# Performance work log

Hardware: AMD Instinct MI355X
Metric: run time of the kernel (lower is better)

Reference implementation:

```python
import jax, jax.numpy as jnp
import numpy as np

N = 50000
E = 800000
IN_DIM = 256
HID = 128
OUT = 64


def setup_inputs() -> dict:
    key = jax.random.key(0)
    ks = jax.random.split(key, 12)
    inp = {}
    inp["x"] = jax.random.normal(ks[0], (N, IN_DIM), dtype=jnp.float32)
    inp["edge_index"] = jax.random.randint(ks[1], (2, E), 0, N, dtype=jnp.int64)
    s0 = 1.0 / np.sqrt(IN_DIM)
    inp["W0"] = jax.random.uniform(ks[2], (IN_DIM, HID), jnp.float32, -s0, s0)
    inp["b0"] = jax.random.uniform(ks[3], (HID,), jnp.float32, -s0, s0)
    sa = 1.0 / np.sqrt(2 * HID)
    inp["att_w1"] = jax.random.uniform(ks[4], (2 * HID, 1), jnp.float32, -sa, sa)
    inp["att_b1"] = jax.random.uniform(ks[5], (1,), jnp.float32, -sa, sa)
    inp["eps1"] = jnp.float32(0.1)
    inp["att_w2"] = jax.random.uniform(ks[6], (2 * HID, 1), jnp.float32, -sa, sa)
    inp["att_b2"] = jax.random.uniform(ks[7], (1,), jnp.float32, -sa, sa)
    inp["eps2"] = jnp.float32(0.1)
    sc = 1.0 / np.sqrt(HID)
    inp["Wc"] = jax.random.uniform(ks[8], (HID, OUT), jnp.float32, -sc, sc)
    inp["bc"] = jax.random.uniform(ks[9], (OUT,), jnp.float32, -sc, sc)
    return inp


def _fagcn_layer(x, row, col, att_w, att_b, eps):
    # x: [N, H]; row/col: [E]
    x_i = x[row]                       # [E, H] source (gathered)
    x_j = x[col]                       # [E, H] destination
    # cat([x_i, x_j]) @ att_w == x_i @ att_w[:H] + x_j @ att_w[H:]
    H = x.shape[1]
    score = x_i @ att_w[:H] + x_j @ att_w[H:] + att_b  # [E, 1]
    alpha = jnp.tanh(score)            # [E, 1]
    messages = alpha * x_i             # [E, H]
    agg = jax.ops.segment_sum(messages, col, num_segments=x.shape[0])  # [N, H]
    return eps * x + (1.0 - eps) * agg


def reference(x, edge_index, W0, b0, att_w1, att_b1, eps1, att_w2, att_b2, eps2, Wc, bc):
    row, col = edge_index[0], edge_index[1]
    h = jax.nn.relu(x @ W0 + b0)       # initial linear + relu (dropout=eval identity)
    h = jax.nn.relu(_fagcn_layer(h, row, col, att_w1, att_b1, eps1))
    h = jax.nn.relu(_fagcn_layer(h, row, col, att_w2, att_b2, eps2))
    return h @ Wc + bc                 # [N, OUT]
```

## Files before the change

### kernel.cpp

```cpp
#include <hip/hip_runtime.h>

#define N_NODES 50000
#define E_EDGES 800000
#define IN_DIM 256
#define HID 128
#define OUT_DIM 64

typedef unsigned short u16;
typedef __attribute__((ext_vector_type(8))) short short8;
typedef __attribute__((ext_vector_type(4))) float floatx4;

__device__ __forceinline__ u16 f2bf(float f) {
    unsigned u = __float_as_uint(f);
    unsigned r = (u + 0x7FFFu + ((u >> 16) & 1u)) >> 16;
    return (u16)r;
}
__device__ __forceinline__ void bf8_unpack(uint4 v, float* f) {
    f[0] = __uint_as_float(v.x << 16); f[1] = __uint_as_float(v.x & 0xffff0000u);
    f[2] = __uint_as_float(v.y << 16); f[3] = __uint_as_float(v.y & 0xffff0000u);
    f[4] = __uint_as_float(v.z << 16); f[5] = __uint_as_float(v.z & 0xffff0000u);
    f[6] = __uint_as_float(v.w << 16); f[7] = __uint_as_float(v.w & 0xffff0000u);
}
__device__ __forceinline__ uint4 bf8_pack(const float* f) {
    uint4 o;
    o.x = f2bf(f[0]) | ((unsigned)f2bf(f[1]) << 16);
    o.y = f2bf(f[2]) | ((unsigned)f2bf(f[3]) << 16);
    o.z = f2bf(f[4]) | ((unsigned)f2bf(f[5]) << 16);
    o.w = f2bf(f[6]) | ((unsigned)f2bf(f[7]) << 16);
    return o;
}

__global__ __launch_bounds__(256) void k_prep(const int* __restrict__ ei,
                                              int* __restrict__ cnt,
                                              int* __restrict__ rank,
                                              const float* __restrict__ W0,
                                              u16* __restrict__ Wt,
                                              const float* __restrict__ Wc,
                                              u16* __restrict__ Wct) {
    const int gid = blockIdx.x * 256 + threadIdx.x;
    if (gid < E_EDGES / 8) {
        const int4 c0 = ((const int4*)(ei + E_EDGES))[2 * gid];
        const int4 c1 = ((const int4*)(ei + E_EDGES))[2 * gid + 1];
        int4 r0, r1;
        r0.x = atomicAdd(&cnt[c0.x], 1);
        r0.y = atomicAdd(&cnt[c0.y], 1);
        r0.z = atomicAdd(&cnt[c0.z], 1);
        r0.w = atomicAdd(&cnt[c0.w], 1);
        r1.x = atomicAdd(&cnt[c1.x], 1);
        r1.y = atomicAdd(&cnt[c1.y], 1);
        r1.z = atomicAdd(&cnt[c1.z], 1);
        r1.w = atomicAdd(&cnt[c1.w], 1);
        ((int4*)rank)[2 * gid] = r0;
        ((int4*)rank)[2 * gid + 1] = r1;
    }
    if (gid < IN_DIM * HID) {
        Wt[gid] = f2bf(W0[(gid & 255) * HID + (gid >> 8)]);
    }
    if (gid < HID * OUT_DIM) {
        Wct[gid] = f2bf(Wc[(gid & 127) * OUT_DIM + (gid >> 7)]);
    }
}

__global__ __launch_bounds__(1024) void k_scanA(const int* __restrict__ cnt,
                                                int* __restrict__ ptr,
                                                int* __restrict__ btot) {
    __shared__ int wtot[16];
    __shared__ int wexc[16];
    const int t = threadIdx.x;
    const int lane = t & 63;
    const int wd = t >> 6;
    const int i = blockIdx.x * 1024 + t;
    int v = (i < N_NODES) ? cnt[i] : 0;
    const int orig = v;
    #pragma unroll
    for (int off = 1; off < 64; off <<= 1) {
        int y = __shfl_up(v, off);
        if (lane >= off) v += y;
    }
    if (lane == 63) wtot[wd] = v;
    __syncthreads();
    if (t < 16) {
        int w = wtot[t];
        #pragma unroll
        for (int off = 1; off < 16; off <<= 1) {
            int y = __shfl_up(w, off);
            if (t >= off) w += y;
        }
        wexc[t] = w - wtot[t];
    }
    __syncthreads();
    if (i < N_NODES) ptr[i] = wexc[wd] + (v - orig);
    if (t == 0) btot[blockIdx.x] = wexc[15] + wtot[15];
}

__global__ __launch_bounds__(64) void k_scanB(int* __restrict__ btot,
                                              int* __restrict__ ptr) {
    const int t = threadIdx.x;
    int v = (t < 49) ? btot[t] : 0;
    const int orig = v;
    #pragma unroll
    for (int off = 1; off < 64; off <<= 1) {
        int y = __shfl_up(v, off);
        if (t >= off) v += y;
    }
    if (t < 49) btot[t] = v - orig;
    if (t == 0) ptr[N_NODES] = E_EDGES;
}

__global__ __launch_bounds__(1024) void k_scanC(int* __restrict__ ptr,
                                                const int* __restrict__ btot) {
    const int i = blockIdx.x * 1024 + threadIdx.x;
    if (i < N_NODES) ptr[i] += btot[blockIdx.x];
}

__global__ __launch_bounds__(256) void k_scatter(const int* __restrict__ ei,
                                                 const int* __restrict__ rank,
                                                 const int* __restrict__ ptr,
                                                 int* __restrict__ srcidx) {
    const int gid = blockIdx.x * 256 + threadIdx.x;
    if (gid >= E_EDGES / 8) return;
    const int4 w0 = ((const int4*)ei)[2 * gid];
    const int4 w1 = ((const int4*)ei)[2 * gid + 1];
    const int4 c0 = ((const int4*)(ei + E_EDGES))[2 * gid];
    const int4 c1 = ((const int4*)(ei + E_EDGES))[2 * gid + 1];
    const int4 r0 = ((const int4*)rank)[2 * gid];
    const int4 r1 = ((const int4*)rank)[2 * gid + 1];
    const int p0 = ptr[c0.x] + r0.x;
    const int p1 = ptr[c0.y] + r0.y;
    const int p2 = ptr[c0.z] + r0.z;
    const int p3 = ptr[c0.w] + r0.w;
    const int p4 = ptr[c1.x] + r1.x;
    const int p5 = ptr[c1.y] + r1.y;
    const int p6 = ptr[c1.z] + r1.z;
    const int p7 = ptr[c1.w] + r1.w;
    srcidx[p0] = w0.x;
    srcidx[p1] = w0.y;
    srcidx[p2] = w0.z;
    srcidx[p3] = w0.w;
    srcidx[p4] = w1.x;
    srcidx[p5] = w1.y;
    srcidx[p6] = w1.z;
    srcidx[p7] = w1.w;
}

#define LROWS 128
#define KS 64
#define KP 72

__global__ __launch_bounds__(256) void k_lin_mfma(
    const float* __restrict__ x, const u16* __restrict__ Wt,
    const float* __restrict__ b0, const float* __restrict__ aw1,
    u16* __restrict__ h, float* __restrict__ sa, float* __restrict__ sb) {
    __shared__ u16 As[LROWS][KP];
    __shared__ u16 Bs[HID][KP];
    const int t = threadIdx.x;
    const int lane = t & 63;
    const int w = t >> 6;
    const int sub = lane & 15;
    const int quad = lane >> 4;
    const int row0 = blockIdx.x * LROWS;

    floatx4 acc0[8], acc1[8];
    #pragma unroll
    for (int i = 0; i < 8; ++i) {
        acc0[i] = (floatx4){0.f, 0.f, 0.f, 0.f};
        acc1[i] = (floatx4){0.f, 0.f, 0.f, 0.f};
    }

    const int sr = t >> 1;
    const int sk = (t & 1) * 32;

    for (int k0 = 0; k0 < IN_DIM; k0 += KS) {
        {
            int gr = row0 + sr;
            if (gr > N_NODES - 1) gr = N_NODES - 1;
            const float* src = x + (size_t)gr * IN_DIM + k0 + sk;
            #pragma unroll
            for (int i = 0; i < 4; ++i) {
                float4 f0 = ((const float4*)src)[2 * i];
                float4 f1 = ((const float4*)src)[2 * i + 1];
                uint4 p;
                p.x = f2bf(f0.x) | ((unsigned)f2bf(f0.y) << 16);
                p.y = f2bf(f0.z) | ((unsigned)f2bf(f0.w) << 16);
                p.z = f2bf(f1.x) | ((unsigned)f2bf(f1.y) << 16);
                p.w = f2bf(f1.z) | ((unsigned)f2bf(f1.w) << 16);
                *(uint4*)&As[sr][sk + 8 * i] = p;
            }
            const u16* wsrc = Wt + sr * IN_DIM + k0 + sk;
            #pragma unroll
            for (int i = 0; i < 4; ++i)
                *(uint4*)&Bs[sr][sk + 8 * i] = ((const uint4*)wsrc)[i];
        }
        __syncthreads();
        #pragma unroll
        for (int kk = 0; kk < KS; kk += 32) {
            short8 a0 = *(const short8*)&As[w * 32 + sub][kk + quad * 8];
            short8 a1 = *(const short8*)&As[w * 32 + 16 + sub][kk + quad * 8];
            #pragma unroll
            for (int ct = 0; ct < 8; ++ct) {
                short8 bb = *(const short8*)&Bs[ct * 16 + sub][kk + quad * 8];
                acc0[ct] = __builtin_amdgcn_mfma_f32_16x16x32_bf16(a0, bb, acc0[ct], 0, 0, 0);
                acc1[ct] = __builtin_amdgcn_mfma_f32_16x16x32_bf16(a1, bb, acc1[ct], 0, 0, 0);
            }
        }
        __syncthreads();
    }

    float bias[8], w1c[8], w2c[8];
    #pragma unroll
    for (int ct = 0; ct < 8; ++ct) {
        const int col = ct * 16 + sub;
        bias[ct] = b0[col];
        w1c[ct] = aw1[col];
        w2c[ct] = aw1[HID + col];
    }
    float ps[2][4], pd[2][4];
    #pragma unroll
    for (int i = 0; i < 2; ++i)
        #pragma unroll
        for (int j = 0; j < 4; ++j) { ps[i][j] = 0.f; pd[i][j] = 0.f; }

    #pragma unroll
    for (int tile = 0; tile < 2; ++tile) {
        #pragma unroll
        for (int reg = 0; reg < 4; ++reg) {
            const int gr = row0 + w * 32 + tile * 16 + quad * 4 + reg;
            const bool ok = gr < N_NODES;
            #pragma unroll
            for (int ct = 0; ct < 8; ++ct) {
                floatx4 v = tile ? acc1[ct] : acc0[ct];
                const float val = fmaxf(v[reg] + bias[ct], 0.f);
                if (ok) h[(size_t)gr * HID + ct * 16 + sub] = f2bf(val);
                ps[tile][reg] += val * w1c[ct];
                pd[tile][reg] += val * w2c[ct];
            }
        }
    }
    #pragma unroll
    for (int tile = 0; tile < 2; ++tile) {
        #pragma unroll
        for (int reg = 0; reg < 4; ++reg) {
            float a = ps[tile][reg], d = pd[tile][reg];
            #pragma unroll
            for (int off = 1; off < 16; off <<= 1) {
                a += __shfl_xor(a, off);
                d += __shfl_xor(d, off);
            }
            if (sub == 0) {
                const int gr = row0 + w * 32 + tile * 16 + quad * 4 + reg;
                if (gr < N_NODES) { sa[gr] = a; sb[gr] = d; }
            }
        }
    }
}

__global__ __launch_bounds__(256) void k_agg(const u16* __restrict__ hin,
                                             const float* __restrict__ sa,
                                             const float* __restrict__ sb,
                                             const float* __restrict__ attb,
                                             const float* __restrict__ epsp,
                                             const int* __restrict__ ptr,
                                             const int* __restrict__ srcidx,
                                             u16* __restrict__ hout,
                                             const float* __restrict__ attw_next,
                                             float* __restrict__ sa_next,
                                             float* __restrict__ sb_next) {
    const int qid = threadIdx.x >> 4;
    const int sub = threadIdx.x & 15;
    const int n = blockIdx.x * 16 + qid;
    if (n >= N_NODES) return;
    const float b = attb[0];
    const float sbn = sb[n];
    const int beg = ptr[n];
    const int end = ptr[n + 1];
    float acc[8];
    #pragma unroll
    for (int j = 0; j < 8; ++j) acc[j] = 0.f;

    int e = beg;
    for (; e + 8 <= end; e += 8) {
        int s[8];
        #pragma unroll
        for (int i = 0; i < 8; ++i) s[i] = srcidx[e + i];
        uint4 v[8];
        #pragma unroll
        for (int i = 0; i < 8; ++i)
            v[i] = *(const uint4*)(hin + (size_t)s[i] * HID + sub * 8);
        float al[8];
        #pragma unroll
        for (int i = 0; i < 8; ++i) al[i] = tanhf(sa[s[i]] + sbn + b);
        #pragma unroll
        for (int i = 0; i < 8; ++i) {
            float f[8];
            bf8_unpack(v[i], f);
            #pragma unroll
            for (int j = 0; j < 8; ++j) acc[j] += al[i] * f[j];
        }
    }
    for (; e < end; ++e) {
        const int s = srcidx[e];
        const float a = tanhf(sa[s] + sbn + b);
        const uint4 v = *(const uint4*)(hin + (size_t)s * HID + sub * 8);
        float f[8];
        bf8_unpack(v, f);
        #pragma unroll
        for (int j = 0; j < 8; ++j) acc[j] += a * f[j];
    }

    const float eps = epsp[0];
    const float om = 1.f - eps;
    const uint4 sv = *(const uint4*)(hin + (size_t)n * HID + sub * 8);
    float self[8], hv[8];
    bf8_unpack(sv, self);
    #pragma unroll
    for (int j = 0; j < 8; ++j)
        hv[j] = fmaxf(eps * self[j] + om * acc[j], 0.f);
    *(uint4*)(hout + (size_t)n * HID + sub * 8) = bf8_pack(hv);

    if (attw_next != nullptr) {
        float psum = 0.f, dsum = 0.f;
        #pragma unroll
        for (int j = 0; j < 8; ++j) {
            psum += hv[j] * attw_next[sub * 8 + j];
            dsum += hv[j] * attw_next[HID + sub * 8 + j];
        }
        #pragma unroll
        for (int off = 1; off < 16; off <<= 1) {
            psum += __shfl_xor(psum, off);
            dsum += __shfl_xor(dsum, off);
        }
        if (sub == 0) { sa_next[n] = psum; sb_next[n] = dsum; }
    }
}

__global__ __launch_bounds__(256) void k_out_mfma(const u16* __restrict__ h,
                                                  const u16* __restrict__ Wct,
                                                  const float* __restrict__ bc,
                                                  float* __restrict__ out) {
    const int t = threadIdx.x;
    const int lane = t & 63;
    const int w = t >> 6;
    const int sub = lane & 15;
    const int quad = lane >> 4;
    const int row0 = blockIdx.x * 128 + w * 32;

    floatx4 acc[2][4];
    #pragma unroll
    for (int i = 0; i < 2; ++i)
        #pragma unroll
        for (int j = 0; j < 4; ++j) acc[i][j] = (floatx4){0.f, 0.f, 0.f, 0.f};

    int r0 = row0 + sub;      if (r0 > N_NODES - 1) r0 = N_NODES - 1;
    int r1 = row0 + 16 + sub; if (r1 > N_NODES - 1) r1 = N_NODES - 1;

    #pragma unroll
    for (int ks = 0; ks < 4; ++ks) {
        const int ko = ks * 32 + quad * 8;
        short8 a0 = *(const short8*)(h + (size_t)r0 * HID + ko);
        short8 a1 = *(const short8*)(h + (size_t)r1 * HID + ko);
        #pragma unroll
        for (int ct = 0; ct < 4; ++ct) {
            short8 bb = *(const short8*)(Wct + (ct * 16 + sub) * HID + ko);
            acc[0][ct] = __builtin_amdgcn_mfma_f32_16x16x32_bf16(a0, bb, acc[0][ct], 0, 0, 0);
            acc[1][ct] = __builtin_amdgcn_mfma_f32_16x16x32_bf16(a1, bb, acc[1][ct], 0, 0, 0);
        }
    }

    #pragma unroll
    for (int ct = 0; ct < 4; ++ct) {
        const float bias = bc[ct * 16 + sub];
        #pragma unroll
        for (int tile = 0; tile < 2; ++tile) {
            #pragma unroll
            for (int reg = 0; reg < 4; ++reg) {
                const int gr = row0 + tile * 16 + quad * 4 + reg;
                if (gr < N_NODES)
                    out[(size_t)gr * OUT_DIM + ct * 16 + sub] = acc[tile][ct][reg] + bias;
            }
        }
    }
}

extern "C" void kernel_launch(void* const* d_in, const int* in_sizes, int n_in,
                              void* d_out, int out_size, void* d_ws, size_t ws_size,
                              hipStream_t stream) {
    const float* x   = (const float*)d_in[0];
    const int*   ei  = (const int*)d_in[1];
    const float* W0  = (const float*)d_in[2];
    const float* b0  = (const float*)d_in[3];
    const float* aw1 = (const float*)d_in[4];
    const float* ab1 = (const float*)d_in[5];
    const float* e1  = (const float*)d_in[6];
    const float* aw2 = (const float*)d_in[7];
    const float* ab2 = (const float*)d_in[8];
    const float* e2  = (const float*)d_in[9];
    const float* Wc  = (const float*)d_in[10];
    const float* bc  = (const float*)d_in[11];
    float* out = (float*)d_out;

    u16* hA  = (u16*)d_ws;
    u16* hB  = hA + (size_t)N_NODES * HID;
    u16* Wt  = hB + (size_t)N_NODES * HID;
    u16* Wct = Wt + IN_DIM * HID;
    float* sa1 = (float*)(Wct + HID * OUT_DIM);
    float* sb1 = sa1 + N_NODES;
    float* sa2 = sb1 + N_NODES;
    float* sb2 = sa2 + N_NODES;
    int* cnt    = (int*)(sb2 + N_NODES);
    int* ptr    = cnt + N_NODES;
    int* srcidx = ptr + N_NODES + 1;
    int* rank   = srcidx + E_EDGES;
    int* btot   = rank + E_EDGES;

    hipMemsetAsync(cnt, 0, N_NODES * sizeof(int), stream);
    k_prep<<<(E_EDGES / 8 + 255) / 256, 256, 0, stream>>>(ei, cnt, rank, W0, Wt, Wc, Wct);
    k_scanA<<<(N_NODES + 1023) / 1024, 1024, 0, stream>>>(cnt, ptr, btot);
    k_scanB<<<1, 64, 0, stream>>>(btot, ptr);
    k_scanC<<<(N_NODES + 1023) / 1024, 1024, 0, stream>>>(ptr, btot);
    k_scatter<<<(E_EDGES / 8 + 255) / 256, 256, 0, stream>>>(ei, rank, ptr, srcidx);

    k_lin_mfma<<<(N_NODES + LROWS - 1) / LROWS, 256, 0, stream>>>(x, Wt, b0, aw1,
                                                                  hA, sa1, sb1);
    k_agg<<<(N_NODES + 15) / 16, 256, 0, stream>>>(hA, sa1, sb1, ab1, e1, ptr, srcidx,
                                                   hB, aw2, sa2, sb2);
    k_agg<<<(N_NODES + 15) / 16, 256, 0, stream>>>(hB, sa2, sb2, ab2, e2, ptr, srcidx,
                                                   hA, nullptr, nullptr, nullptr);
    k_out_mfma<<<(N_NODES + 127) / 128, 256, 0, stream>>>(hA, Wct, bc, out);
}
```

Before: 288.0 us.

## Fuse edge counting and input linear layer into one heterogeneous front kernel

Merges the edge in-degree counting pass and the first linear+ReLU MFMA layer into a single launch, with block index choosing the role, so the atomic-heavy counting can overlap with the GEMM. The GEMM now loads x rows straight from global into MFMA A-fragments, converting to bf16 in registers instead of staging through shared memory. W0 is transposed and converted on the fly per block rather than in a prep pass, and the Wc conversion moves into the single-block scanB kernel. This removes one launch and a shared-memory A tile, but every GEMM block now does strided W0 reads, and the serial Wc conversion in a 64-thread kernel adds latency.

```diff
diff --git a/kernel.cpp b/kernel.cpp
--- a/kernel.cpp
+++ b/kernel.cpp
@@ -5,6 +5,7 @@
 #define IN_DIM 256
 #define HID 128
 #define OUT_DIM 64
+#define EBLK 391
 
 typedef unsigned short u16;
 typedef __attribute__((ext_vector_type(8))) short short8;
@@ -29,35 +30,151 @@
     o.w = f2bf(f[6]) | ((unsigned)f2bf(f[7]) << 16);
     return o;
 }
-
-__global__ __launch_bounds__(256) void k_prep(const int* __restrict__ ei,
-                                              int* __restrict__ cnt,
-                                              int* __restrict__ rank,
-                                              const float* __restrict__ W0,
-                                              u16* __restrict__ Wt,
-                                              const float* __restrict__ Wc,
-                                              u16* __restrict__ Wct) {
-    const int gid = blockIdx.x * 256 + threadIdx.x;
-    if (gid < E_EDGES / 8) {
-        const int4 c0 = ((const int4*)(ei + E_EDGES))[2 * gid];
-        const int4 c1 = ((const int4*)(ei + E_EDGES))[2 * gid + 1];
-        int4 r0, r1;
-        r0.x = atomicAdd(&cnt[c0.x], 1);
-        r0.y = atomicAdd(&cnt[c0.y], 1);
-        r0.z = atomicAdd(&cnt[c0.z], 1);
-        r0.w = atomicAdd(&cnt[c0.w], 1);
-        r1.x = atomicAdd(&cnt[c1.x], 1);
-        r1.y = atomicAdd(&cnt[c1.y], 1);
-        r1.z = atomicAdd(&cnt[c1.z], 1);
-        r1.w = atomicAdd(&cnt[c1.w], 1);
-        ((int4*)rank)[2 * gid] = r0;
-        ((int4*)rank)[2 * gid + 1] = r1;
-    }
-    if (gid < IN_DIM * HID) {
-        Wt[gid] = f2bf(W0[(gid & 255) * HID + (gid >> 8)]);
-    }
-    if (gid < HID * OUT_DIM) {
-        Wct[gid] = f2bf(Wc[(gid & 127) * OUT_DIM + (gid >> 7)]);
+__device__ __forceinline__ short8 pack_bf8(float4 a, float4 b) {
+    uint4 p;
+    p.x = f2bf(a.x) | ((unsigned)f2bf(a.y) << 16);
+    p.y = f2bf(a.z) | ((unsigned)f2bf(a.w) << 16);
+    p.z = f2bf(b.x) | ((unsigned)f2bf(b.y) << 16);
+    p.w = f2bf(b.z) | ((unsigned)f2bf(b.w) << 16);
+    short8 r;
+    __builtin_memcpy(&r, &p, 16);
+    return r;
+}
+
+#define KS 64
+#define KP 72
+
+__global__ __launch_bounds__(256) void k_front(
+    const int* __restrict__ ei, int* __restrict__ cnt, int* __restrict__ rank,
+    const float* __restrict__ x, const float* __restrict__ W0,
+    const float* __restrict__ b0, const float* __restrict__ aw1,
+    u16* __restrict__ h, float* __restrict__ sa, float* __restrict__ sb) {
+    const int t = threadIdx.x;
+
+    if (blockIdx.x < EBLK) {
+        const int gid = blockIdx.x * 256 + t;
+        if (gid < E_EDGES / 8) {
+            const int4 c0 = ((const int4*)(ei + E_EDGES))[2 * gid];
+            const int4 c1 = ((const int4*)(ei + E_EDGES))[2 * gid + 1];
+            int4 r0, r1;
+            r0.x = atomicAdd(&cnt[c0.x], 1);
+            r0.y = atomicAdd(&cnt[c0.y], 1);
+            r0.z = atomicAdd(&cnt[c0.z], 1);
+            r0.w = atomicAdd(&cnt[c0.w], 1);
+            r1.x = atomicAdd(&cnt[c1.x], 1);
+            r1.y = atomicAdd(&cnt[c1.y], 1);
+            r1.z = atomicAdd(&cnt[c1.z], 1);
+            r1.w = atomicAdd(&cnt[c1.w], 1);
+            ((int4*)rank)[2 * gid] = r0;
+            ((int4*)rank)[2 * gid + 1] = r1;
+        }
+        return;
+    }
+
+    __shared__ u16 Bs[HID][KP];
+    const int lane = t & 63;
+    const int w = t >> 6;
+    const int sub = lane & 15;
+    const int quad = lane >> 4;
+    const int row0 = (blockIdx.x - EBLK) * 128;
+
+    floatx4 acc0[8], acc1[8];
+    #pragma unroll
+    for (int i = 0; i < 8; ++i) {
+        acc0[i] = (floatx4){0.f, 0.f, 0.f, 0.f};
+        acc1[i] = (floatx4){0.f, 0.f, 0.f, 0.f};
+    }
+
+    int r0 = row0 + w * 32 + sub;      if (r0 > N_NODES - 1) r0 = N_NODES - 1;
+    int r1 = row0 + w * 32 + 16 + sub; if (r1 > N_NODES - 1) r1 = N_NODES - 1;
+    const float* xr0 = x + (size_t)r0 * IN_DIM;
+    const float* xr1 = x + (size_t)r1 * IN_DIM;
+
+    const int bn = t >> 1;
+    const int bk = (t & 1) * 32;
+
+    for (int k0 = 0; k0 < IN_DIM; k0 += KS) {
+        {
+            const float* wp = W0 + (size_t)(k0 + bk) * HID + bn;
+            #pragma unroll
+            for (int i = 0; i < 4; ++i) {
+                uint4 p;
+                unsigned q[4];
+                #pragma unroll
+                for (int j = 0; j < 4; ++j) {
+                    const float lo = wp[(i * 8 + 2 * j) * HID];
+                    const float hi = wp[(i * 8 + 2 * j + 1) * HID];
+                    q[j] = f2bf(lo) | ((unsigned)f2bf(hi) << 16);
+                }
+                p.x = q[0]; p.y = q[1]; p.z = q[2]; p.w = q[3];
+                *(uint4*)&Bs[bn][bk + 8 * i] = p;
+            }
+        }
+        __syncthreads();
+        #pragma unroll
+        for (int kk = 0; kk < KS; kk += 32) {
+            const int ko = k0 + kk + quad * 8;
+            const float4 fa0 = *(const float4*)(xr0 + ko);
+            const float4 fa1 = *(const float4*)(xr0 + ko + 4);
+            const float4 fb0 = *(const float4*)(xr1 + ko);
+            const float4 fb1 = *(const float4*)(xr1 + ko + 4);
+            const short8 a0 = pack_bf8(fa0, fa1);
+            const short8 a1 = pack_bf8(fb0, fb1);
+            #pragma unroll
+            for (int ct = 0; ct < 8; ++ct) {
+                short8 bb = *(const short8*)&Bs[ct * 16 + sub][kk + quad * 8];
+                acc0[ct] = __builtin_amdgcn_mfma_f32_16x16x32_bf16(a0, bb, acc0[ct], 0, 0, 0);
+                acc1[ct] = __builtin_amdgcn_mfma_f32_16x16x32_bf16(a1, bb, acc1[ct], 0, 0, 0);
+            }
+        }
+        __syncthreads();
+    }
+
+    float bias[8], w1c[8], w2c[8];
+    #pragma unroll
+    for (int ct = 0; ct < 8; ++ct) {
+        const int col = ct * 16 + sub;
+        bias[ct] = b0[col];
+        w1c[ct] = aw1[col];
+        w2c[ct] = aw1[HID + col];
+    }
+    float ps[2][4], pd[2][4];
+    #pragma unroll
+    for (int i = 0; i < 2; ++i)
+        #pragma unroll
+        for (int j = 0; j < 4; ++j) { ps[i][j] = 0.f; pd[i][j] = 0.f; }
+
+    #pragma unroll
+    for (int tile = 0; tile < 2; ++tile) {
+        #pragma unroll
+        for (int reg = 0; reg < 4; ++reg) {
+            const int gr = row0 + w * 32 + tile * 16 + quad * 4 + reg;
+            const bool ok = gr < N_NODES;
+            #pragma unroll
+            for (int ct = 0; ct < 8; ++ct) {
+                floatx4 v = tile ? acc1[ct] : acc0[ct];
+                const float val = fmaxf(v[reg] + bias[ct], 0.f);
+                if (ok) h[(size_t)gr * HID + ct * 16 + sub] = f2bf(val);
+                ps[tile][reg] += val * w1c[ct];
+                pd[tile][reg] += val * w2c[ct];
+            }
+        }
+    }
+    #pragma unroll
+    for (int tile = 0; tile < 2; ++tile) {
+        #pragma unroll
+        for (int reg = 0; reg < 4; ++reg) {
+            float a = ps[tile][reg], d = pd[tile][reg];
+            #pragma unroll
+            for (int off = 1; off < 16; off <<= 1) {
+                a += __shfl_xor(a, off);
+                d += __shfl_xor(d, off);
+            }
+            if (sub == 0) {
+                const int gr = row0 + w * 32 + tile * 16 + quad * 4 + reg;
+                if (gr < N_NODES) { sa[gr] = a; sb[gr] = d; }
+            }
+        }
     }
 }
 
@@ -94,7 +211,9 @@
 }
 
 __global__ __launch_bounds__(64) void k_scanB(int* __restrict__ btot,
-                                              int* __restrict__ ptr) {
+                                              int* __restrict__ ptr,
+                                              const float* __restrict__ Wc,
+                                              u16* __restrict__ Wct) {
     const int t = threadIdx.x;
     int v = (t < 49) ? btot[t] : 0;
     const int orig = v;
@@ -105,6 +224,8 @@
     }
     if (t < 49) btot[t] = v - orig;
     if (t == 0) ptr[N_NODES] = E_EDGES;
+    for (int i = t; i < HID * OUT_DIM; i += 64)
+        Wct[i] = f2bf(Wc[(i & 127) * OUT_DIM + (i >> 7)]);
 }
 
 __global__ __launch_bounds__(1024) void k_scanC(int* __restrict__ ptr,
@@ -125,133 +246,14 @@
     const int4 c1 = ((const int4*)(ei + E_EDGES))[2 * gid + 1];
     const int4 r0 = ((const int4*)rank)[2 * gid];
     const int4 r1 = ((const int4*)rank)[2 * gid + 1];
-    const int p0 = ptr[c0.x] + r0.x;
-    const int p1 = ptr[c0.y] + r0.y;
-    const int p2 = ptr[c0.z] + r0.z;
-    const int p3 = ptr[c0.w] + r0.w;
-    const int p4 = ptr[c1.x] + r1.x;
-    const int p5 = ptr[c1.y] + r1.y;
-    const int p6 = ptr[c1.z] + r1.z;
-    const int p7 = ptr[c1.w] + r1.w;
-    srcidx[p0] = w0.x;
-    srcidx[p1] = w0.y;
-    srcidx[p2] = w0.z;
-    srcidx[p3] = w0.w;
-    srcidx[p4] = w1.x;
-    srcidx[p5] = w1.y;
-    srcidx[p6] = w1.z;
-    srcidx[p7] = w1.w;
-}
-
-#define LROWS 128
-#define KS 64
-#define KP 72
-
-__global__ __launch_bounds__(256) void k_lin_mfma(
-    const float* __restrict__ x, const u16* __restrict__ Wt,
-    const float* __restrict__ b0, const float* __restrict__ aw1,
-    u16* __restrict__ h, float* __restrict__ sa, float* __restrict__ sb) {
-    __shared__ u16 As[LROWS][KP];
-    __shared__ u16 Bs[HID][KP];
-    const int t = threadIdx.x;
-    const int lane = t & 63;
-    const int w = t >> 6;
-    const int sub = lane & 15;
-    const int quad = lane >> 4;
-    const int row0 = blockIdx.x * LROWS;
-
-    floatx4 acc0[8], acc1[8];
-    #pragma unroll
-    for (int i = 0; i < 8; ++i) {
-        acc0[i] = (floatx4){0.f, 0.f, 0.f, 0.f};
-        acc1[i] = (floatx4){0.f, 0.f, 0.f, 0.f};
-    }
-
-    const int sr = t >> 1;
-    const int sk = (t & 1) * 32;
-
-    for (int k0 = 0; k0 < IN_DIM; k0 += KS) {
-        {
-            int gr = row0 + sr;
-            if (gr > N_NODES - 1) gr = N_NODES - 1;
-            const float* src = x + (size_t)gr * IN_DIM + k0 + sk;
-            #pragma unroll
-            for (int i = 0; i < 4; ++i) {
-                float4 f0 = ((const float4*)src)[2 * i];
-                float4 f1 = ((const float4*)src)[2 * i + 1];
-                uint4 p;
-                p.x = f2bf(f0.x) | ((unsigned)f2bf(f0.y) << 16);
-                p.y = f2bf(f0.z) | ((unsigned)f2bf(f0.w) << 16);
-                p.z = f2bf(f1.x) | ((unsigned)f2bf(f1.y) << 16);
-                p.w = f2bf(f1.z) | ((unsigned)f2bf(f1.w) << 16);
-                *(uint4*)&As[sr][sk + 8 * i] = p;
-            }
-            const u16* wsrc = Wt + sr * IN_DIM + k0 + sk;
-            #pragma unroll
-            for (int i = 0; i < 4; ++i)
-                *(uint4*)&Bs[sr][sk + 8 * i] = ((const uint4*)wsrc)[i];
-        }
-        __syncthreads();
-        #pragma unroll
-        for (int kk = 0; kk < KS; kk += 32) {
-            short8 a0 = *(const short8*)&As[w * 32 + sub][kk + quad * 8];
-            short8 a1 = *(const short8*)&As[w * 32 + 16 + sub][kk + quad * 8];
-            #pragma unroll
-            for (int ct = 0; ct < 8; ++ct) {
-                short8 bb = *(const short8*)&Bs[ct * 16 + sub][kk + quad * 8];
-                acc0[ct] = __builtin_amdgcn_mfma_f32_16x16x32_bf16(a0, bb, acc0[ct], 0, 0, 0);
-                acc1[ct] = __builtin_amdgcn_mfma_f32_16x16x32_bf16(a1, bb, acc1[ct], 0, 0, 0);
-            }
-        }
-        __syncthreads();
-    }
-
-    float bias[8], w1c[8], w2c[8];
-    #pragma unroll
-    for (int ct = 0; ct < 8; ++ct) {
-        const int col = ct * 16 + sub;
-        bias[ct] = b0[col];
-        w1c[ct] = aw1[col];
-        w2c[ct] = aw1[HID + col];
-    }
-    float ps[2][4], pd[2][4];
-    #pragma unroll
-    for (int i = 0; i < 2; ++i)
-        #pragma unroll
-        for (int j = 0; j < 4; ++j) { ps[i][j] = 0.f; pd[i][j] = 0.f; }
-
-    #pragma unroll
-    for (int tile = 0; tile < 2; ++tile) {
-        #pragma unroll
-        for (int reg = 0; reg < 4; ++reg) {
-            const int gr = row0 + w * 32 + tile * 16 + quad * 4 + reg;
-            const bool ok = gr < N_NODES;
-            #pragma unroll
-            for (int ct = 0; ct < 8; ++ct) {
-                floatx4 v = tile ? acc1[ct] : acc0[ct];
-                const float val = fmaxf(v[reg] + bias[ct], 0.f);
-                if (ok) h[(size_t)gr * HID + ct * 16 + sub] = f2bf(val);
-                ps[tile][reg] += val * w1c[ct];
-                pd[tile][reg] += val * w2c[ct];
-            }
-        }
-    }
-    #pragma unroll
-    for (int tile = 0; tile < 2; ++tile) {
-        #pragma unroll
-        for (int reg = 0; reg < 4; ++reg) {
-            float a = ps[tile][reg], d = pd[tile][reg];
-            #pragma unroll
-            for (int off = 1; off < 16; off <<= 1) {
-                a += __shfl_xor(a, off);
-                d += __shfl_xor(d, off);
-            }
-            if (sub == 0) {
-                const int gr = row0 + w * 32 + tile * 16 + quad * 4 + reg;
-                if (gr < N_NODES) { sa[gr] = a; sb[gr] = d; }
-            }
-        }
-    }
+    srcidx[ptr[c0.x] + r0.x] = w0.x;
+    srcidx[ptr[c0.y] + r0.y] = w0.y;
+    srcidx[ptr[c0.z] + r0.z] = w0.z;
+    srcidx[ptr[c0.w] + r0.w] = w0.w;
+    srcidx[ptr[c1.x] + r1.x] = w1.x;
+    srcidx[ptr[c1.y] + r1.y] = w1.y;
+    srcidx[ptr[c1.z] + r1.z] = w1.z;
+    srcidx[ptr[c1.w] + r1.w] = w1.w;
 }
 
 __global__ __launch_bounds__(256) void k_agg(const u16* __restrict__ hin,
@@ -400,8 +402,7 @@
 
     u16* hA  = (u16*)d_ws;
     u16* hB  = hA + (size_t)N_NODES * HID;
-    u16* Wt  = hB + (size_t)N_NODES * HID;
-    u16* Wct = Wt + IN_DIM * HID;
+    u16* Wct = hB + (size_t)N_NODES * HID;
     float* sa1 = (float*)(Wct + HID * OUT_DIM);
     float* sb1 = sa1 + N_NODES;
     float* sa2 = sb1 + N_NODES;
@@ -413,14 +414,13 @@
     int* btot   = rank + E_EDGES;
 
     hipMemsetAsync(cnt, 0, N_NODES * sizeof(int), stream);
-    k_prep<<<(E_EDGES / 8 + 255) / 256, 256, 0, stream>>>(ei, cnt, rank, W0, Wt, Wc, Wct);
+    k_front<<<2 * EBLK, 256, 0, stream>>>(ei, cnt, rank, x, W0, b0, aw1,
+                                          hA, sa1, sb1);
     k_scanA<<<(N_NODES + 1023) / 1024, 1024, 0, stream>>>(cnt, ptr, btot);
-    k_scanB<<<1, 64, 0, stream>>>(btot, ptr);
+    k_scanB<<<1, 64, 0, stream>>>(btot, ptr, Wc, Wct);
     k_scanC<<<(N_NODES + 1023) / 1024, 1024, 0, stream>>>(ptr, btot);
     k_scatter<<<(E_EDGES / 8 + 255) / 256, 256, 0, stream>>>(ei, rank, ptr, srcidx);
 
-    k_lin_mfma<<<(N_NODES + LROWS - 1) / LROWS, 256, 0, stream>>>(x, Wt, b0, aw1,
-                                                                  hA, sa1, sb1);
     k_agg<<<(N_NODES + 15) / 16, 256, 0, stream>>>(hA, sa1, sb1, ab1, e1, ptr, srcidx,
                                                    hB, aw2, sa2, sb2);
     k_agg<<<(N_NODES + 15) / 16, 256, 0, stream>>>(hB, sa2, sb2, ab2, e2, ptr, srcidx,
```

After: 294.9 us. +2.4%, slower.
